# Kernel optimization log

Measured on AMD Instinct MI355X. Metric: run time of the kernel, lower is better.

## Reference

```python
import jax, jax.numpy as jnp
import numpy as np

TEMPERATURE = 0.5


def setup_inputs() -> dict:
    key = jax.random.key(0)
    k1, k2 = jax.random.split(key)
    N, Z = 4096, 2048
    z1 = jax.random.normal(k1, (N, Z), dtype=jnp.float32)
    z2 = jax.random.normal(k2, (N, Z), dtype=jnp.float32)
    return {"z1": z1, "z2": z2}


def reference(z1, z2):
    # NT-Xent loss. Original torch code: normalize, build full 2Nx2N cosine-sim
    # matrix, prepend the positive pair column, cross-entropy with label 0.
    # Mathematically, per-row CE with the positive prepended and the self-sim
    # removed equals: logsumexp over the row excluding the diagonal, minus the
    # positive logit.  (cosine_similarity on already-normalized vectors is a
    # plain dot product, so normalization is applied once.)
    n, _ = z1.shape
    a = z1 / jnp.linalg.norm(z1, axis=1, keepdims=True)  # [N, Z]
    b = z2 / jnp.linalg.norm(z2, axis=1, keepdims=True)  # [N, Z]
    reps = jnp.concatenate([a, b], axis=0)               # [2N, Z]
    logits = jnp.matmul(reps, reps.T) / TEMPERATURE      # [2N, 2N]
    NEG_INF = jnp.float32(-1e9)  # mask self-similarity (excluded from CE denom)
    logits = jnp.where(jnp.eye(2 * n, dtype=bool), NEG_INF, logits)
    pos = jnp.sum(a * b, axis=1) / TEMPERATURE           # [N] positive logits
    pos = jnp.concatenate([pos, pos])                    # [2N]
    lse = jax.nn.logsumexp(logits, axis=1)               # [2N]
    # sum of CE over 2N rows, divided by 2N  == mean
    return jnp.mean(lse - pos)
```

## Files before the change

kernel.cpp:

```cpp
#include <hip/hip_runtime.h>
#include <stdint.h>

#define N_ROWS 4096
#define Z_DIM  2048
#define TOT    8192
#define RBYTES (Z_DIM / 2)
#define BKE    128
#define KBYT   (BKE / 2)
#define NITER  (Z_DIM / BKE)
#define BM     256
#define BN     128
#define NBLK   1056
#define ABYTES (BM * KBYT)
#define BUFB   (ABYTES + BN * KBYT)
#define INV_T  2.0f
#define SCL4   64.0f

typedef __attribute__((ext_vector_type(4))) int   intx4;
typedef __attribute__((ext_vector_type(8))) int   intx8;
typedef __attribute__((ext_vector_type(4))) float floatx4;

#define GLOAD16(g, l)                                                   \
    __builtin_amdgcn_global_load_lds(                                   \
        (const __attribute__((address_space(1))) unsigned int*)(g),     \
        (__attribute__((address_space(3))) unsigned int*)(l), 16, 0, 0)

__device__ __forceinline__ unsigned int f2fp4(float v) {
    float a = fabsf(v);
    unsigned int c = (a >= 0.25f) + (a >= 0.75f) + (a >= 1.25f) + (a >= 1.75f)
                   + (a >= 2.5f)  + (a >= 3.5f)  + (a >= 5.0f);
    return c | (v < 0.f ? 8u : 0u);
}

__global__ __launch_bounds__(256) void normalize_kernel(
    const float* __restrict__ z1, const float* __restrict__ z2,
    unsigned char* __restrict__ reps, float* __restrict__ pos,
    float* __restrict__ rowsum)
{
    const int row  = blockIdx.x;
    const int tid  = threadIdx.x;
    const int lane = tid & 63, wave = tid >> 6;

    if (row < TOT / 256) rowsum[row * 256 + tid] = 0.f;

    const float4* p1 = (const float4*)(z1 + (size_t)row * Z_DIM);
    const float4* p2 = (const float4*)(z2 + (size_t)row * Z_DIM);
    float4 x0 = p1[tid * 2], x1 = p1[tid * 2 + 1];
    float4 y0 = p2[tid * 2], y1 = p2[tid * 2 + 1];

    float s1 = x0.x*x0.x + x0.y*x0.y + x0.z*x0.z + x0.w*x0.w
             + x1.x*x1.x + x1.y*x1.y + x1.z*x1.z + x1.w*x1.w;
    float s2 = y0.x*y0.x + y0.y*y0.y + y0.z*y0.z + y0.w*y0.w
             + y1.x*y1.x + y1.y*y1.y + y1.z*y1.z + y1.w*y1.w;
    float dd = x0.x*y0.x + x0.y*y0.y + x0.z*y0.z + x0.w*y0.w
             + x1.x*y1.x + x1.y*y1.y + x1.z*y1.z + x1.w*y1.w;

    #pragma unroll
    for (int m = 1; m < 64; m <<= 1) {
        s1 += __shfl_xor(s1, m);
        s2 += __shfl_xor(s2, m);
        dd += __shfl_xor(dd, m);
    }
    __shared__ float red[3][4];
    if (lane == 0) { red[0][wave] = s1; red[1][wave] = s2; red[2][wave] = dd; }
    __syncthreads();
    s1 = red[0][0] + red[0][1] + red[0][2] + red[0][3];
    s2 = red[1][0] + red[1][1] + red[1][2] + red[1][3];
    dd = red[2][0] + red[2][1] + red[2][2] + red[2][3];

    const float inv1 = rsqrtf(s1), inv2 = rsqrtf(s2);
    if (tid == 0) {
        float p = dd * inv1 * inv2 * INV_T;
        pos[row] = p;
        pos[row + N_ROWS] = p;
    }

    const float a = inv1 * SCL4, b = inv2 * SCL4;
    unsigned int pa =  f2fp4(x0.x * a)        | (f2fp4(x0.y * a) << 4)
                    | (f2fp4(x0.z * a) << 8)  | (f2fp4(x0.w * a) << 12)
                    | (f2fp4(x1.x * a) << 16) | (f2fp4(x1.y * a) << 20)
                    | (f2fp4(x1.z * a) << 24) | (f2fp4(x1.w * a) << 28);
    unsigned int pb =  f2fp4(y0.x * b)        | (f2fp4(y0.y * b) << 4)
                    | (f2fp4(y0.z * b) << 8)  | (f2fp4(y0.w * b) << 12)
                    | (f2fp4(y1.x * b) << 16) | (f2fp4(y1.y * b) << 20)
                    | (f2fp4(y1.z * b) << 24) | (f2fp4(y1.w * b) << 28);
    *(unsigned int*)(reps + (size_t)row * RBYTES + tid * 4) = pa;
    *(unsigned int*)(reps + (size_t)(N_ROWS + row) * RBYTES + tid * 4) = pb;
}

__global__ __launch_bounds__(256, 2) void simclr_gemm(
    const unsigned char* __restrict__ reps, float* __restrict__ rowsum)
{
    __shared__ __align__(16) unsigned char L[3 * BUFB];

    const int t = blockIdx.x;
    int ri = (int)((65.0f - sqrtf(4225.0f - 4.0f * (float)t)) * 0.5f);
    while (ri * (65 - ri) > t) --ri;
    while ((ri + 1) * (64 - ri) <= t) ++ri;
    const int cj = 2 * ri + (t - ri * (65 - ri));

    const int row0 = ri * BM;
    const int col0 = cj * BN;

    const int tid  = threadIdx.x;
    const int lane = tid & 63, wave = tid >> 6;
    const int wr = wave >> 1, wc = wave & 1;
    const int quad = lane >> 4, l16 = lane & 15;

    const bool deadW = (cj == 2 * ri) && (wr == 1);

    const unsigned char* gsrc[6];
    int lofs[6];
    #pragma unroll
    for (int c = 0; c < 6; ++c) {
        const int m   = wave * 384 + c * 64 + lane;
        const int opB = (m >= ABYTES / 16);
        const int mm  = opB ? m - ABYTES / 16 : m;
        const int gr  = (opB ? col0 : row0) + (mm >> 2);
        gsrc[c] = reps + (size_t)gr * RBYTES + (mm & 3) * 16;
        lofs[c] = m * 16;
    }

    floatx4 acc[8][4];
    #pragma unroll
    for (int i = 0; i < 8; ++i)
        #pragma unroll
        for (int j = 0; j < 4; ++j)
            acc[i][j] = floatx4{0.f, 0.f, 0.f, 0.f};

    #pragma unroll
    for (int c = 0; c < 6; ++c) GLOAD16(gsrc[c],        &L[lofs[c]]);
    #pragma unroll
    for (int c = 0; c < 6; ++c) GLOAD16(gsrc[c] + KBYT, &L[BUFB + lofs[c]]);

    int cur = 0;
    #pragma unroll 1
    for (int i = 0; i < NITER; ++i) {
        if (i + 1 < NITER) asm volatile("s_waitcnt vmcnt(6)" ::: "memory");
        else               asm volatile("s_waitcnt vmcnt(0)" ::: "memory");
        __builtin_amdgcn_s_barrier();
        asm volatile("" ::: "memory");

        if (i + 2 < NITER) {
            int pf = cur + 2; if (pf >= 3) pf -= 3;
            unsigned char* Lp = &L[pf * BUFB];
            const int ko = (i + 2) * KBYT;
            #pragma unroll
            for (int c = 0; c < 6; ++c) GLOAD16(gsrc[c] + ko, Lp + lofs[c]);
        }

        if (!deadW) {
            const unsigned char* Lc = &L[cur * BUFB];
            intx8 b8[4];
            #pragma unroll
            for (int j = 0; j < 4; ++j) {
                intx4 bv = *(const intx4*)(Lc + ABYTES
                             + (wc * 64 + j * 16 + l16) * KBYT + quad * 16);
                b8[j] = intx8{bv[0], bv[1], bv[2], bv[3], 0, 0, 0, 0};
            }
            #pragma unroll
            for (int fi = 0; fi < 8; ++fi) {
                intx4 av = *(const intx4*)(Lc
                             + (wr * 128 + fi * 16 + l16) * KBYT + quad * 16);
                intx8 a8 = intx8{av[0], av[1], av[2], av[3], 0, 0, 0, 0};
                __builtin_amdgcn_s_setprio(1);
                #pragma unroll
                for (int j = 0; j < 4; ++j)
                    acc[fi][j] = __builtin_amdgcn_mfma_scale_f32_16x16x128_f8f6f4(
                        a8, b8[j], acc[fi][j],
                        4, 4,
                        0, 0x7F7F7F7Fu,
                        0, 0x7F7F7F7Fu);
                __builtin_amdgcn_s_setprio(0);
            }
        }
        cur = (cur == 2) ? 0 : cur + 1;
    }

    const float descale = INV_T / (SCL4 * SCL4);
    if (!deadW) {
        float scol[4] = {0.f, 0.f, 0.f, 0.f};
        #pragma unroll
        for (int fi = 0; fi < 8; ++fi) {
            const int rbase = row0 + wr * 128 + fi * 16 + quad * 4;
            float srow[4] = {0.f, 0.f, 0.f, 0.f};
            #pragma unroll
            for (int j = 0; j < 4; ++j) {
                const int c = col0 + wc * 64 + j * 16 + l16;
                #pragma unroll
                for (int rr = 0; rr < 4; ++rr) {
                    float e = (c > rbase + rr)
                            ? __expf(acc[fi][j][rr] * descale) : 0.f;
                    srow[rr] += e;
                    scol[j]  += e;
                }
            }
            #pragma unroll
            for (int rr = 0; rr < 4; ++rr) {
                #pragma unroll
                for (int m = 1; m < 16; m <<= 1)
                    srow[rr] += __shfl_xor(srow[rr], m);
            }
            if (l16 == 0) {
                #pragma unroll
                for (int rr = 0; rr < 4; ++rr)
                    atomicAdd(&rowsum[rbase + rr], srow[rr]);
            }
        }
        #pragma unroll
        for (int j = 0; j < 4; ++j) {
            scol[j] += __shfl_xor(scol[j], 16);
            scol[j] += __shfl_xor(scol[j], 32);
        }
        if (quad == 0) {
            #pragma unroll
            for (int j = 0; j < 4; ++j)
                atomicAdd(&rowsum[col0 + wc * 64 + j * 16 + l16], scol[j]);
        }
    }
}

__global__ __launch_bounds__(1024) void finalize_kernel(
    const float* __restrict__ rowsum, const float* __restrict__ pos,
    float* __restrict__ out)
{
    const int tid = threadIdx.x;
    const int lane = tid & 63, wave = tid >> 6;
    float s = 0.f;
    for (int r = tid; r < TOT; r += 1024) s += logf(rowsum[r]) - pos[r];
    #pragma unroll
    for (int m = 1; m < 64; m <<= 1) s += __shfl_xor(s, m);
    __shared__ float red[16];
    if (lane == 0) red[wave] = s;
    __syncthreads();
    if (tid == 0) {
        float t = 0.f;
        #pragma unroll
        for (int w = 0; w < 16; ++w) t += red[w];
        out[0] = t * (1.0f / TOT);
    }
}

extern "C" void kernel_launch(void* const* d_in, const int* in_sizes, int n_in,
                              void* d_out, int out_size, void* d_ws, size_t ws_size,
                              hipStream_t stream)
{
    const float* z1 = (const float*)d_in[0];
    const float* z2 = (const float*)d_in[1];
    float* out = (float*)d_out;

    char* w = (char*)d_ws;
    unsigned char* reps = (unsigned char*)w;
    float* pos    = (float*)(w + (size_t)TOT * RBYTES);
    float* rowsum = pos + TOT;

    normalize_kernel<<<N_ROWS, 256, 0, stream>>>(z1, z2, reps, pos, rowsum);
    simclr_gemm<<<NBLK, 256, 0, stream>>>(reps, rowsum);
    finalize_kernel<<<1, 1024, 0, stream>>>(rowsum, pos, out);
}
```

Measured before the change: 170.5 us.

## Use 256x256 tiles with 512 threads, swizzled LDS, and interleaved loads

```diff
diff --git a/kernel.cpp b/kernel.cpp
--- a/kernel.cpp
+++ b/kernel.cpp
@@ -9,10 +9,11 @@
 #define KBYT   (BKE / 2)
 #define NITER  (Z_DIM / BKE)
 #define BM     256
-#define BN     128
-#define NBLK   1056
-#define ABYTES (BM * KBYT)
-#define BUFB   (ABYTES + BN * KBYT)
+#define BN     256
+#define NT32   (TOT / BM)
+#define NBLK   528
+#define OPB    (BM * KBYT)
+#define BUFB   (2 * OPB)
 #define INV_T  2.0f
 #define SCL4   64.0f
 
@@ -88,38 +89,36 @@
     *(unsigned int*)(reps + (size_t)(N_ROWS + row) * RBYTES + tid * 4) = pb;
 }
 
-__global__ __launch_bounds__(256, 2) void simclr_gemm(
+__global__ __launch_bounds__(512, 2) void simclr_gemm(
     const unsigned char* __restrict__ reps, float* __restrict__ rowsum)
 {
     __shared__ __align__(16) unsigned char L[3 * BUFB];
 
     const int t = blockIdx.x;
-    int ri = (int)((65.0f - sqrtf(4225.0f - 4.0f * (float)t)) * 0.5f);
-    while (ri * (65 - ri) > t) --ri;
-    while ((ri + 1) * (64 - ri) <= t) ++ri;
-    const int cj = 2 * ri + (t - ri * (65 - ri));
-
-    const int row0 = ri * BM;
-    const int col0 = cj * BN;
+    int ri = (int)((65.0f - sqrtf(4225.0f - 8.0f * (float)t)) * 0.5f);
+    while (ri > 0  && ri * 32 - ri * (ri - 1) / 2 > t) --ri;
+    while (ri < 31 && (ri + 1) * 32 - (ri + 1) * ri / 2 <= t) ++ri;
+    const int cj = ri + (t - (ri * 32 - ri * (ri - 1) / 2));
+    const bool diag = (ri == cj);
+    const int row0 = ri * BM, col0 = cj * BN;
 
     const int tid  = threadIdx.x;
     const int lane = tid & 63, wave = tid >> 6;
-    const int wr = wave >> 1, wc = wave & 1;
+    const int wr = wave >> 2, wc = wave & 3;
     const int quad = lane >> 4, l16 = lane & 15;
 
-    const bool deadW = (cj == 2 * ri) && (wr == 1);
-
-    const unsigned char* gsrc[6];
-    int lofs[6];
-    #pragma unroll
-    for (int c = 0; c < 6; ++c) {
-        const int m   = wave * 384 + c * 64 + lane;
-        const int opB = (m >= ABYTES / 16);
-        const int mm  = opB ? m - ABYTES / 16 : m;
-        const int gr  = (opB ? col0 : row0) + (mm >> 2);
-        gsrc[c] = reps + (size_t)gr * RBYTES + (mm & 3) * 16;
-        lofs[c] = m * 16;
-    }
+    const bool alive = !(diag && wr == 1 && wc < 2);
+
+    const unsigned char* gsrc[4];
+    #pragma unroll
+    for (int q = 0; q < 4; ++q) {
+        const int rl = (q & 1) * 128 + (tid >> 2);
+        const int g  = (tid & 3) ^ ((rl >> 1) & 3);
+        const int rowg = (q < 2 ? row0 : col0) + rl;
+        gsrc[q] = reps + (size_t)rowg * RBYTES + g * 16;
+    }
+    const int dstoff = tid * 16;
+    const int swz = (quad ^ ((l16 >> 1) & 3)) << 4;
 
     floatx4 acc[8][4];
     #pragma unroll
@@ -129,56 +128,74 @@
             acc[i][j] = floatx4{0.f, 0.f, 0.f, 0.f};
 
     #pragma unroll
-    for (int c = 0; c < 6; ++c) GLOAD16(gsrc[c],        &L[lofs[c]]);
-    #pragma unroll
-    for (int c = 0; c < 6; ++c) GLOAD16(gsrc[c] + KBYT, &L[BUFB + lofs[c]]);
+    for (int q = 0; q < 4; ++q) GLOAD16(gsrc[q],        &L[0 * BUFB + q * 8192 + dstoff]);
+    #pragma unroll
+    for (int q = 0; q < 4; ++q) GLOAD16(gsrc[q] + KBYT, &L[1 * BUFB + q * 8192 + dstoff]);
 
     int cur = 0;
     #pragma unroll 1
     for (int i = 0; i < NITER; ++i) {
-        if (i + 1 < NITER) asm volatile("s_waitcnt vmcnt(6)" ::: "memory");
+        if (i + 1 < NITER) asm volatile("s_waitcnt vmcnt(4)" ::: "memory");
         else               asm volatile("s_waitcnt vmcnt(0)" ::: "memory");
         __builtin_amdgcn_s_barrier();
-        asm volatile("" ::: "memory");
-
-        if (i + 2 < NITER) {
-            int pf = cur + 2; if (pf >= 3) pf -= 3;
-            unsigned char* Lp = &L[pf * BUFB];
-            const int ko = (i + 2) * KBYT;
-            #pragma unroll
-            for (int c = 0; c < 6; ++c) GLOAD16(gsrc[c] + ko, Lp + lofs[c]);
-        }
-
-        if (!deadW) {
-            const unsigned char* Lc = &L[cur * BUFB];
-            intx8 b8[4];
-            #pragma unroll
-            for (int j = 0; j < 4; ++j) {
-                intx4 bv = *(const intx4*)(Lc + ABYTES
-                             + (wc * 64 + j * 16 + l16) * KBYT + quad * 16);
-                b8[j] = intx8{bv[0], bv[1], bv[2], bv[3], 0, 0, 0, 0};
-            }
-            #pragma unroll
-            for (int fi = 0; fi < 8; ++fi) {
-                intx4 av = *(const intx4*)(Lc
-                             + (wr * 128 + fi * 16 + l16) * KBYT + quad * 16);
-                intx8 a8 = intx8{av[0], av[1], av[2], av[3], 0, 0, 0, 0};
-                __builtin_amdgcn_s_setprio(1);
-                #pragma unroll
-                for (int j = 0; j < 4; ++j)
-                    acc[fi][j] = __builtin_amdgcn_mfma_scale_f32_16x16x128_f8f6f4(
-                        a8, b8[j], acc[fi][j],
-                        4, 4,
-                        0, 0x7F7F7F7Fu,
-                        0, 0x7F7F7F7Fu);
-                __builtin_amdgcn_s_setprio(0);
-            }
-        }
+
+        int pf = cur + 2; if (pf >= 3) pf -= 3;
+        const bool st = (i + 2 < NITER);
+        const size_t ko = (size_t)(i + 2) * KBYT;
+        const unsigned char* Ab = &L[cur * BUFB];
+        const unsigned char* Bb = Ab + OPB;
+        unsigned char* Lp = &L[pf * BUFB];
+
+        intx8 b8[4];
+
+#define PHASE(p)                                                             \
+        {                                                                    \
+            intx4 a0v, a1v;                                                  \
+            if (alive) {                                                     \
+                if (p == 0) {                                                \
+                    _Pragma("unroll")                                        \
+                    for (int j = 0; j < 4; ++j) {                            \
+                        const int rb = wc * 64 + j * 16 + l16;               \
+                        intx4 bv = *(const intx4*)(Bb + rb * KBYT + swz);    \
+                        b8[j] = intx8{bv[0], bv[1], bv[2], bv[3], 0,0,0,0};  \
+                    }                                                        \
+                }                                                            \
+                a0v = *(const intx4*)(Ab + (wr*128 + (2*(p))  *16 + l16)*KBYT + swz); \
+                a1v = *(const intx4*)(Ab + (wr*128 + (2*(p)+1)*16 + l16)*KBYT + swz); \
+            }                                                                \
+            if (st) GLOAD16(gsrc[p] + ko, Lp + (p) * 8192 + dstoff);         \
+            __builtin_amdgcn_s_barrier();                                    \
+            if (alive) {                                                     \
+                intx8 a80 = intx8{a0v[0], a0v[1], a0v[2], a0v[3], 0,0,0,0};  \
+                intx8 a81 = intx8{a1v[0], a1v[1], a1v[2], a1v[3], 0,0,0,0};  \
+                __builtin_amdgcn_s_setprio(1);                               \
+                _Pragma("unroll")                                            \
+                for (int j = 0; j < 4; ++j)                                  \
+                    acc[2*(p)][j] =                                          \
+                        __builtin_amdgcn_mfma_scale_f32_16x16x128_f8f6f4(    \
+                            a80, b8[j], acc[2*(p)][j],                       \
+                            4, 4, 0, 0x7F7F7F7Fu, 0, 0x7F7F7F7Fu);           \
+                _Pragma("unroll")                                            \
+                for (int j = 0; j < 4; ++j)                                  \
+                    acc[2*(p)+1][j] =                                        \
+                        __builtin_amdgcn_mfma_scale_f32_16x16x128_f8f6f4(    \
+                            a81, b8[j], acc[2*(p)+1][j],                     \
+                            4, 4, 0, 0x7F7F7F7Fu, 0, 0x7F7F7F7Fu);           \
+                __builtin_amdgcn_s_setprio(0);                               \
+            }                                                                \
+        }
+
+        PHASE(0)
+        PHASE(1)
+        PHASE(2)
+        PHASE(3)
+#undef PHASE
+
         cur = (cur == 2) ? 0 : cur + 1;
     }
 
     const float descale = INV_T / (SCL4 * SCL4);
-    if (!deadW) {
+    if (alive) {
         float scol[4] = {0.f, 0.f, 0.f, 0.f};
         #pragma unroll
         for (int fi = 0; fi < 8; ++fi) {
@@ -189,7 +206,7 @@
                 const int c = col0 + wc * 64 + j * 16 + l16;
                 #pragma unroll
                 for (int rr = 0; rr < 4; ++rr) {
-                    float e = (c > rbase + rr)
+                    float e = (!diag || c > rbase + rr)
                             ? __expf(acc[fi][j][rr] * descale) : 0.f;
                     srow[rr] += e;
                     scol[j]  += e;
@@ -255,6 +272,6 @@
     float* rowsum = pos + TOT;
 
     normalize_kernel<<<N_ROWS, 256, 0, stream>>>(z1, z2, reps, pos, rowsum);
-    simclr_gemm<<<NBLK, 256, 0, stream>>>(reps, rowsum);
+    simclr_gemm<<<NBLK, 512, 0, stream>>>(reps, rowsum);
     finalize_kernel<<<1, 1024, 0, stream>>>(rowsum, pos, out);
 }
```

Result: slower. 174.4 us (+2.3%).
